# Kernel optimization log

Measured on AMD Instinct MI355X. Metric: run time of the kernel, lower is better.

Reference implementation:

```python
import jax, jax.numpy as jnp
import numpy as np

E = 1024
FF = 4096
B, S = 4, 2048
EPS = 1e-5

def _layernorm(x, g, b):
    m = jnp.mean(x, axis=-1, keepdims=True)
    v = jnp.var(x, axis=-1, keepdims=True)
    return (x - m) * jax.lax.rsqrt(v + EPS) * g + b

def setup_inputs() -> dict:
    key = jax.random.key(0)
    ks = jax.random.split(key, 16)
    def lin(k, fan_in, shape):
        bound = 1.0 / np.sqrt(fan_in)
        return jax.random.uniform(k, shape, jnp.float32, -bound, bound)
    return {
        "src_embs": jax.random.normal(ks[0], (B, S, E), jnp.float32),
        "Wq_w": lin(ks[1], E, (E, E)), "Wq_b": lin(ks[2], E, (E,)),
        "Wk_w": lin(ks[3], E, (E, E)), "Wk_b": lin(ks[4], E, (E,)),
        "Wv_w": lin(ks[5], E, (E, E)), "Wv_b": lin(ks[6], E, (E,)),
        "Wo_w": lin(ks[7], E, (E, E)), "Wo_b": lin(ks[8], E, (E,)),
        "W1_w": lin(ks[9], E, (FF, E)), "W1_b": lin(ks[10], E, (FF,)),
        "W2_w": lin(ks[11], FF, (E, FF)), "W2_b": lin(ks[12], FF, (E,)),
        "g1": jnp.ones((E,), jnp.float32), "b1": jnp.zeros((E,), jnp.float32),
        "g2": jnp.ones((E,), jnp.float32), "b2": jnp.zeros((E,), jnp.float32),
        "g3": jnp.ones((E,), jnp.float32), "b3": jnp.zeros((E,), jnp.float32),
    }

def reference(src_embs, Wq_w, Wq_b, Wk_w, Wk_b, Wv_w, Wv_b, Wo_w, Wo_b,
              W1_w, W1_b, W2_w, W2_b, g1, b1, g2, b2, g3, b3):
    x = _layernorm(src_embs, g1, b1)
    Q = x @ Wq_w.T + Wq_b
    K = x @ Wk_w.T + Wk_b
    V = x @ Wv_w.T + Wv_b
    # single-head attention, scaled by sqrt(embed_dim) per source
    scores = jnp.einsum('bqe,bke->bqk', Q, K) / jnp.sqrt(jnp.float32(E))
    attn = jax.nn.softmax(scores, axis=-1)
    attn_out = jnp.einsum('bqk,bke->bqe', attn, V) @ Wo_w.T + Wo_b
    h = src_embs + attn_out
    hn = _layernorm(h, g2, b2)
    ff = jax.nn.relu(hn @ W1_w.T + W1_b) @ W2_w.T + W2_b
    out = h + ff
    return _layernorm(out, g3, b3)
```

## Files before the change

kernel.cpp:

```cpp
#include <hip/hip_runtime.h>
#include <cstdint>
#include <cmath>

#define E_DIM 1024
#define FF_DIM 4096
#define B_DIM 4
#define S_DIM 2048
#define NTOK (B_DIM * S_DIM)
#define QKV_N 3072

typedef __bf16 bf16;
typedef __attribute__((ext_vector_type(8))) __bf16 bf16x8;
typedef __attribute__((ext_vector_type(4))) float f32x4;

__device__ __forceinline__ void gload_lds16(const void* g, void* l) {
  __builtin_amdgcn_global_load_lds(
      (const __attribute__((address_space(1))) unsigned int*)g,
      (__attribute__((address_space(3))) unsigned int*)l, 16, 0, 0);
}

__device__ __forceinline__ float waveRedSum(float v) {
#pragma unroll
  for (int o = 32; o > 0; o >>= 1) v += __shfl_xor(v, o, 64);
  return v;
}
__device__ __forceinline__ float waveRedMax(float v) {
#pragma unroll
  for (int o = 32; o > 0; o >>= 1) v = fmaxf(v, __shfl_xor(v, o, 64));
  return v;
}

__global__ __launch_bounds__(256) void cvt_k(const float* __restrict__ in,
                                             bf16* __restrict__ out, int n4) {
  int i = blockIdx.x * 256 + threadIdx.x;
  if (i < n4) {
    float4 v = reinterpret_cast<const float4*>(in)[i];
    bf16* o = out + (size_t)i * 4;
    o[0] = (bf16)v.x; o[1] = (bf16)v.y; o[2] = (bf16)v.z; o[3] = (bf16)v.w;
  }
}

template <typename OutT>
__global__ __launch_bounds__(256) void layernorm_k(const float* __restrict__ x,
                                                   OutT* __restrict__ out,
                                                   const float* __restrict__ g,
                                                   const float* __restrict__ b) {
  const int row = blockIdx.x;
  const int tid = threadIdx.x;
  const float4 v = reinterpret_cast<const float4*>(x + (size_t)row * E_DIM)[tid];
  float s = v.x + v.y + v.z + v.w;
  float q = v.x * v.x + v.y * v.y + v.z * v.z + v.w * v.w;
  s = waveRedSum(s);
  q = waveRedSum(q);
  __shared__ float sa[4], sb[4];
  const int lane = tid & 63, wid = tid >> 6;
  if (lane == 0) { sa[wid] = s; sb[wid] = q; }
  __syncthreads();
  s = sa[0] + sa[1] + sa[2] + sa[3];
  q = sb[0] + sb[1] + sb[2] + sb[3];
  const float mean = s * (1.0f / E_DIM);
  const float var = q * (1.0f / E_DIM) - mean * mean;
  const float rstd = rsqrtf(var + 1e-5f);
  const int c = tid * 4;
  OutT* op = out + (size_t)row * E_DIM + c;
  const float vv[4] = {v.x, v.y, v.z, v.w};
#pragma unroll
  for (int j = 0; j < 4; ++j)
    op[j] = (OutT)((vv[j] - mean) * rstd * g[c + j] + b[c + j]);
}

__global__ __launch_bounds__(256) void softmax_k(bf16* __restrict__ scores) {
  const int row = blockIdx.x;
  bf16* rp = scores + (size_t)row * S_DIM;
  const int tid = threadIdx.x;
  const int lane = tid & 63, wid = tid >> 6;
  bf16x8 v8 = *reinterpret_cast<const bf16x8*>(rp + tid * 8);
  float v[8];
#pragma unroll
  for (int j = 0; j < 8; ++j) v[j] = (float)v8[j];
  float mx = v[0];
#pragma unroll
  for (int j = 1; j < 8; ++j) mx = fmaxf(mx, v[j]);
  mx = waveRedMax(mx);
  __shared__ float sm_[4], ss_[4];
  if (lane == 0) sm_[wid] = mx;
  __syncthreads();
  mx = fmaxf(fmaxf(sm_[0], sm_[1]), fmaxf(sm_[2], sm_[3]));
  float e[8];
  float s = 0.f;
#pragma unroll
  for (int j = 0; j < 8; ++j) { e[j] = __expf(v[j] - mx); s += e[j]; }
  s = waveRedSum(s);
  if (lane == 0) ss_[wid] = s;
  __syncthreads();
  s = ss_[0] + ss_[1] + ss_[2] + ss_[3];
  const float inv = 1.0f / s;
  bf16x8 o;
#pragma unroll
  for (int j = 0; j < 8; ++j) o[j] = (bf16)(e[j] * inv);
  *reinterpret_cast<bf16x8*>(rp + tid * 8) = o;
}

__global__ __launch_bounds__(256) void transpose_k(const bf16* __restrict__ in,
                                                   int ld_in, size_t bstride_in,
                                                   bf16* __restrict__ out) {
  __shared__ bf16 t[32][33];
  const int b = blockIdx.z;
  const bf16* ip = in + (size_t)b * bstride_in;
  bf16* op = out + (size_t)b * S_DIM * E_DIM;
  const int e0 = blockIdx.x * 32, s0 = blockIdx.y * 32;
  const int tx = threadIdx.x & 31, ty = threadIdx.x >> 5;
#pragma unroll
  for (int r = 0; r < 32; r += 8)
    t[ty + r][tx] = ip[(size_t)(s0 + ty + r) * ld_in + e0 + tx];
  __syncthreads();
#pragma unroll
  for (int r = 0; r < 32; r += 8)
    op[(size_t)(e0 + ty + r) * S_DIM + s0 + tx] = t[tx][ty + r];
}

template <int BN, typename OutT, bool RELU>
__global__ __launch_bounds__(512) void gemm8p_k(
    const bf16* __restrict__ A0, int lda, const bf16* __restrict__ Bt0, int ldb,
    OutT* __restrict__ C0, int ldc, int M, int N, int K,
    const float* __restrict__ bias, const float* __restrict__ resid, int ldr,
    float scale, size_t sAz, size_t sBz, size_t sCz) {
  constexpr int BM = 256;
  constexpr int WAVE_N = BN / 4;
  constexpr int NPH = (BN == 256) ? 4 : 2;
  constexpr int NHH = (BN == 256) ? 2 : 1;
  constexpr int NCH_B = BN / 64;
  constexpr int NCH = 4 + NCH_B;
  constexpr int CPP = NCH / NPH;
  constexpr int MIDP = (BN == 256) ? 1 : 0;
  constexpr int DBUF = (BM + BN) * 128;
  __shared__ __align__(16) char smem[2 * DBUF];

  const int tid = threadIdx.x;
  const int lane = tid & 63;
  const int wid = tid >> 6;
  const int wr = wid >> 2;
  const int wc = wid & 3;

  const bf16* A = A0 + (size_t)blockIdx.z * sAz;
  const bf16* Bt = Bt0 + (size_t)blockIdx.z * sBz;
  OutT* C = C0 + (size_t)blockIdx.z * sCz;

  const int gx = gridDim.x;
  const int nwg = gx * gridDim.y;
  int wg = blockIdx.y * gx + blockIdx.x;
  {
    const int q = nwg >> 3, r8 = nwg & 7;
    const int xcd = wg & 7, lin = wg >> 3;
    wg = (xcd < r8 ? xcd * (q + 1) : r8 * (q + 1) + (xcd - r8) * q) + lin;
  }
  const int m0 = (wg / gx) * 256;
  const int n0 = (wg % gx) * BN;

  auto stage_chunk = [&](int t, int c) {
    char* base = smem + (t & 1) * DBUF;
    const int r8 = tid >> 3;
    const int gg = tid & 7;
    if (c < NCH_B) {
      const int row = c * 64 + r8;
      const int g = gg ^ (row & 7);
      gload_lds16(Bt + (size_t)(n0 + row) * ldb + t * 64 + g * 8,
                  base + BM * 128 + c * 8192 + wid * 1024);
    } else {
      const int i = c - NCH_B;
      const int ca = ((i & 1) << 1) | (i >> 1);
      const int row = ca * 64 + r8;
      const int g = gg ^ (row & 7);
      gload_lds16(A + (size_t)(m0 + row) * lda + t * 64 + g * 8,
                  base + ca * 8192 + wid * 1024);
    }
  };

  f32x4 acc[2][4][NHH][2] = {};
  bf16x8 af[4][2];
  bf16x8 bfv[NHH][2][2];

  const int NT = K >> 6;
#pragma unroll
  for (int c = 0; c < NCH; ++c) stage_chunk(0, c);
  asm volatile("s_waitcnt vmcnt(2)" ::: "memory");
  __builtin_amdgcn_s_barrier();

  for (int t = 0; t < NT; ++t) {
    const char* lA = smem + (t & 1) * DBUF;
    const char* lB = lA + BM * 128;
#pragma unroll
    for (int p = 0; p < NPH; ++p) {
      const int mh = (BN == 256) ? (p >> 1) : p;
      const int nh = (BN == 256) ? (p & 1) : 0;
      if ((BN == 256) ? (p == 0 || p == 2) : true) {
#pragma unroll
        for (int fm = 0; fm < 4; ++fm) {
          const int row = wr * 128 + mh * 64 + fm * 16 + (lane & 15);
#pragma unroll
          for (int ks = 0; ks < 2; ++ks) {
            const int g = ((ks << 2) | (lane >> 4)) ^ (row & 7);
            af[fm][ks] = *reinterpret_cast<const bf16x8*>(lA + row * 128 + g * 16);
          }
        }
      }
      if (p < NHH) {
#pragma unroll
        for (int fn = 0; fn < 2; ++fn) {
          const int row = wc * WAVE_N + p * 32 + fn * 16 + (lane & 15);
#pragma unroll
          for (int ks = 0; ks < 2; ++ks) {
            const int g = ((ks << 2) | (lane >> 4)) ^ (row & 7);
            bfv[p][fn][ks] =
                *reinterpret_cast<const bf16x8*>(lB + row * 128 + g * 16);
          }
        }
      }
      if (t + 1 < NT) {
#pragma unroll
        for (int c = 0; c < CPP; ++c) stage_chunk(t + 1, p * CPP + c);
      }
      __builtin_amdgcn_s_barrier();
      __builtin_amdgcn_s_setprio(1);
#pragma unroll
      for (int fm = 0; fm < 4; ++fm)
#pragma unroll
        for (int fn = 0; fn < 2; ++fn) {
          acc[mh][fm][nh][fn] = __builtin_amdgcn_mfma_f32_16x16x32_bf16(
              af[fm][0], bfv[nh][fn][0], acc[mh][fm][nh][fn], 0, 0, 0);
          acc[mh][fm][nh][fn] = __builtin_amdgcn_mfma_f32_16x16x32_bf16(
              af[fm][1], bfv[nh][fn][1], acc[mh][fm][nh][fn], 0, 0, 0);
        }
      __builtin_amdgcn_s_setprio(0);
      if (p == MIDP) {
        if (t + 1 < NT) {
          if constexpr (BN == 256) asm volatile("s_waitcnt vmcnt(4)" ::: "memory");
          else                     asm volatile("s_waitcnt vmcnt(3)" ::: "memory");
        } else {
          asm volatile("s_waitcnt vmcnt(0)" ::: "memory");
        }
      }
      if (p == NPH - 1) {
        asm volatile("s_waitcnt vmcnt(2)" ::: "memory");
      }
      __builtin_amdgcn_s_barrier();
    }
  }

#pragma unroll
  for (int mh = 0; mh < 2; ++mh)
#pragma unroll
    for (int nh = 0; nh < NHH; ++nh)
#pragma unroll
      for (int fn = 0; fn < 2; ++fn) {
        const int col = n0 + wc * WAVE_N + nh * 32 + fn * 16 + (lane & 15);
        const float bv = bias ? bias[col] : 0.0f;
#pragma unroll
        for (int fm = 0; fm < 4; ++fm)
#pragma unroll
          for (int i = 0; i < 4; ++i) {
            const int row = m0 + wr * 128 + mh * 64 + fm * 16 + (lane >> 4) * 4 + i;
            float v = acc[mh][fm][nh][fn][i] * scale + bv;
            if (resid) v += resid[(size_t)row * ldr + col];
            if (RELU) v = fmaxf(v, 0.0f);
            C[(size_t)row * ldc + col] = (OutT)v;
          }
      }
}

extern "C" void kernel_launch(void* const* d_in, const int* in_sizes, int n_in,
                              void* d_out, int out_size, void* d_ws,
                              size_t ws_size, hipStream_t stream) {
  const float* src = (const float*)d_in[0];
  const float* Wq_w = (const float*)d_in[1];
  const float* Wq_b = (const float*)d_in[2];
  const float* Wk_w = (const float*)d_in[3];
  const float* Wk_b = (const float*)d_in[4];
  const float* Wv_w = (const float*)d_in[5];
  const float* Wv_b = (const float*)d_in[6];
  const float* Wo_w = (const float*)d_in[7];
  const float* Wo_b = (const float*)d_in[8];
  const float* W1_w = (const float*)d_in[9];
  const float* W1_b = (const float*)d_in[10];
  const float* W2_w = (const float*)d_in[11];
  const float* W2_b = (const float*)d_in[12];
  const float* g1 = (const float*)d_in[13];
  const float* b1 = (const float*)d_in[14];
  const float* g2 = (const float*)d_in[15];
  const float* b2 = (const float*)d_in[16];
  const float* g3 = (const float*)d_in[17];
  const float* b3 = (const float*)d_in[18];
  float* out = (float*)d_out;
  (void)ws_size; (void)in_sizes; (void)n_in; (void)out_size;

  const size_t MB = 1ull << 20;
  char* ws = (char*)d_ws;
  bf16* wqkv = (bf16*)(ws + 0 * MB);
  bf16* wo = (bf16*)(ws + 6 * MB);
  bf16* w1 = (bf16*)(ws + 8 * MB);
  bf16* w2 = (bf16*)(ws + 16 * MB);
  bf16* Cqkv = (bf16*)(ws + 24 * MB);
  bf16* Vt = (bf16*)(ws + 72 * MB);
  bf16* scoresB = (bf16*)(ws + 88 * MB);
  bf16* xln = (bf16*)(ws + 88 * MB);
  float* bqkv = (float*)(ws + 104 * MB);
  bf16* ctx = Cqkv;
  bf16* hn = scoresB;
  bf16* f1 = (bf16*)(ws + 24 * MB);
  float* h = out;

  cvt_k<<<(E_DIM * E_DIM / 4 + 255) / 256, 256, 0, stream>>>(Wq_w, wqkv, E_DIM * E_DIM / 4);
  cvt_k<<<(E_DIM * E_DIM / 4 + 255) / 256, 256, 0, stream>>>(Wk_w, wqkv + (size_t)E_DIM * E_DIM, E_DIM * E_DIM / 4);
  cvt_k<<<(E_DIM * E_DIM / 4 + 255) / 256, 256, 0, stream>>>(Wv_w, wqkv + 2 * (size_t)E_DIM * E_DIM, E_DIM * E_DIM / 4);
  cvt_k<<<(E_DIM * E_DIM / 4 + 255) / 256, 256, 0, stream>>>(Wo_w, wo, E_DIM * E_DIM / 4);
  cvt_k<<<(FF_DIM * E_DIM / 4 + 255) / 256, 256, 0, stream>>>(W1_w, w1, FF_DIM * E_DIM / 4);
  cvt_k<<<(FF_DIM * E_DIM / 4 + 255) / 256, 256, 0, stream>>>(W2_w, w2, FF_DIM * E_DIM / 4);
  hipMemcpyAsync(bqkv, Wq_b, E_DIM * 4, hipMemcpyDeviceToDevice, stream);
  hipMemcpyAsync(bqkv + E_DIM, Wk_b, E_DIM * 4, hipMemcpyDeviceToDevice, stream);
  hipMemcpyAsync(bqkv + 2 * E_DIM, Wv_b, E_DIM * 4, hipMemcpyDeviceToDevice, stream);

  layernorm_k<bf16><<<NTOK, 256, 0, stream>>>(src, xln, g1, b1);

  dim3 gQKV(QKV_N / 256, NTOK / 256);
  gemm8p_k<256, bf16, false><<<gQKV, 512, 0, stream>>>(
      xln, E_DIM, wqkv, E_DIM, Cqkv, QKV_N, NTOK, QKV_N, E_DIM,
      bqkv, nullptr, 0, 1.0f, 0, 0, 0);

  dim3 gSc(S_DIM / 256, S_DIM / 256, B_DIM);
  gemm8p_k<256, bf16, false><<<gSc, 512, 0, stream>>>(
      Cqkv, QKV_N, Cqkv + E_DIM, QKV_N, scoresB, S_DIM, S_DIM, S_DIM, E_DIM,
      nullptr, nullptr, 0, 1.0f / 32.0f,
      (size_t)S_DIM * QKV_N, (size_t)S_DIM * QKV_N, (size_t)S_DIM * S_DIM);

  softmax_k<<<B_DIM * S_DIM, 256, 0, stream>>>(scoresB);

  transpose_k<<<dim3(E_DIM / 32, S_DIM / 32, B_DIM), 256, 0, stream>>>(
      Cqkv + 2 * E_DIM, QKV_N, (size_t)S_DIM * QKV_N, Vt);

  dim3 gPV(E_DIM / 128, S_DIM / 256, B_DIM);
  gemm8p_k<128, bf16, false><<<gPV, 512, 0, stream>>>(
      scoresB, S_DIM, Vt, S_DIM, ctx, E_DIM, S_DIM, E_DIM, S_DIM,
      nullptr, nullptr, 0, 1.0f,
      (size_t)S_DIM * S_DIM, (size_t)S_DIM * E_DIM, (size_t)S_DIM * E_DIM);

  dim3 gWo(E_DIM / 128, NTOK / 256);
  gemm8p_k<128, float, false><<<gWo, 512, 0, stream>>>(
      ctx, E_DIM, wo, E_DIM, h, E_DIM, NTOK, E_DIM, E_DIM,
      Wo_b, src, E_DIM, 1.0f, 0, 0, 0);

  layernorm_k<bf16><<<NTOK, 256, 0, stream>>>(h, hn, g2, b2);

  dim3 gF1(FF_DIM / 256, NTOK / 256);
  gemm8p_k<256, bf16, true><<<gF1, 512, 0, stream>>>(
      hn, E_DIM, w1, E_DIM, f1, FF_DIM, NTOK, FF_DIM, E_DIM,
      W1_b, nullptr, 0, 1.0f, 0, 0, 0);

  dim3 gF2(E_DIM / 128, NTOK / 256);
  gemm8p_k<128, float, false><<<gF2, 512, 0, stream>>>(
      f1, FF_DIM, w2, FF_DIM, out, E_DIM, NTOK, E_DIM, FF_DIM,
      W2_b, h, E_DIM, 1.0f, 0, 0, 0);

  layernorm_k<float><<<NTOK, 256, 0, stream>>>(out, out, g3, b3);
}
```

Baseline: 423.7 us.

## Triple-buffer LDS prefetch pipeline for BN=128 GEMM variant

For the BN=128 GEMM instantiation, the shared-memory staging grows from two buffers to three and loads are issued two K-tiles ahead instead of one, with the vmcnt waits adjusted to match. The goal is to hide more global-to-LDS latency behind the MFMA work. In exchange it uses more LDS per block (3x(256+128)x128 bytes), which may lower occupancy, and the final tiles now drain with vmcnt(0). The BN=256 path keeps its double-buffered schedule.

```diff
diff --git a/kernel.cpp b/kernel.cpp
--- a/kernel.cpp
+++ b/kernel.cpp
@@ -132,9 +132,9 @@
   constexpr int NCH_B = BN / 64;
   constexpr int NCH = 4 + NCH_B;
   constexpr int CPP = NCH / NPH;
-  constexpr int MIDP = (BN == 256) ? 1 : 0;
+  constexpr int DEPTH = (BN == 256) ? 2 : 3;
   constexpr int DBUF = (BM + BN) * 128;
-  __shared__ __align__(16) char smem[2 * DBUF];
+  __shared__ __align__(16) char smem[DEPTH * DBUF];
 
   const int tid = threadIdx.x;
   const int lane = tid & 63;
@@ -158,7 +158,7 @@
   const int n0 = (wg % gx) * BN;
 
   auto stage_chunk = [&](int t, int c) {
-    char* base = smem + (t & 1) * DBUF;
+    char* base = smem + (t % DEPTH) * DBUF;
     const int r8 = tid >> 3;
     const int gg = tid & 7;
     if (c < NCH_B) {
@@ -181,13 +181,21 @@
   bf16x8 bfv[NHH][2][2];
 
   const int NT = K >> 6;
-#pragma unroll
-  for (int c = 0; c < NCH; ++c) stage_chunk(0, c);
-  asm volatile("s_waitcnt vmcnt(2)" ::: "memory");
+  if constexpr (BN == 256) {
+#pragma unroll
+    for (int c = 0; c < NCH; ++c) stage_chunk(0, c);
+    asm volatile("s_waitcnt vmcnt(2)" ::: "memory");
+  } else {
+#pragma unroll
+    for (int c = 0; c < NCH; ++c) stage_chunk(0, c);
+#pragma unroll
+    for (int c = 0; c < NCH; ++c) stage_chunk(1, c);
+    asm volatile("s_waitcnt vmcnt(6)" ::: "memory");
+  }
   __builtin_amdgcn_s_barrier();
 
   for (int t = 0; t < NT; ++t) {
-    const char* lA = smem + (t & 1) * DBUF;
+    const char* lA = smem + (t % DEPTH) * DBUF;
     const char* lB = lA + BM * 128;
 #pragma unroll
     for (int p = 0; p < NPH; ++p) {
@@ -216,9 +224,16 @@
           }
         }
       }
-      if (t + 1 < NT) {
-#pragma unroll
-        for (int c = 0; c < CPP; ++c) stage_chunk(t + 1, p * CPP + c);
+      if constexpr (BN == 256) {
+        if (t + 1 < NT) {
+#pragma unroll
+          for (int c = 0; c < CPP; ++c) stage_chunk(t + 1, p * CPP + c);
+        }
+      } else {
+        if (t + 2 < NT) {
+#pragma unroll
+          for (int c = 0; c < CPP; ++c) stage_chunk(t + 2, p * CPP + c);
+        }
       }
       __builtin_amdgcn_s_barrier();
       __builtin_amdgcn_s_setprio(1);
@@ -232,16 +247,19 @@
               af[fm][1], bfv[nh][fn][1], acc[mh][fm][nh][fn], 0, 0, 0);
         }
       __builtin_amdgcn_s_setprio(0);
-      if (p == MIDP) {
-        if (t + 1 < NT) {
-          if constexpr (BN == 256) asm volatile("s_waitcnt vmcnt(4)" ::: "memory");
-          else                     asm volatile("s_waitcnt vmcnt(3)" ::: "memory");
-        } else {
-          asm volatile("s_waitcnt vmcnt(0)" ::: "memory");
-        }
-      }
-      if (p == NPH - 1) {
-        asm volatile("s_waitcnt vmcnt(2)" ::: "memory");
+      if constexpr (BN == 256) {
+        if (p == 1) {
+          if (t + 1 < NT) asm volatile("s_waitcnt vmcnt(4)" ::: "memory");
+          else            asm volatile("s_waitcnt vmcnt(0)" ::: "memory");
+        }
+        if (p == NPH - 1) {
+          asm volatile("s_waitcnt vmcnt(2)" ::: "memory");
+        }
+      } else {
+        if (p == NPH - 1) {
+          if (t + 2 < NT) asm volatile("s_waitcnt vmcnt(6)" ::: "memory");
+          else            asm volatile("s_waitcnt vmcnt(0)" ::: "memory");
+        }
       }
       __builtin_amdgcn_s_barrier();
     }
```

Measured after the change: 416.9 us. No clear change (-1.6%).
